# Kernel optimization log

Measured on AMD Instinct MI355X. Metric: run time of the kernel, lower is better.

Reference implementation:

```python
import jax, jax.numpy as jnp
import numpy as np

N_NODES = 100000
N_EDGES = 3200000
N_GRAPHS = 2000
F_IN, H, N_CLS = 14, 64, 2


def _glorot(key, shape):
    lim = float(np.sqrt(6.0 / (shape[0] + shape[1])))
    return jax.random.uniform(key, shape, jnp.float32, -lim, lim)


def setup_inputs() -> dict:
    key = jax.random.key(0)
    ks = jax.random.split(key, 16)
    x = jax.random.normal(ks[0], (N_NODES, F_IN), jnp.float32)
    edge_index = jax.random.randint(ks[1], (2, N_EDGES), 0, N_NODES, jnp.int64)
    batch = jnp.sort(jax.random.randint(ks[2], (N_NODES,), 0, N_GRAPHS, jnp.int64))
    return {
        "x": x,
        "W1l": _glorot(ks[3], (F_IN, H)), "W1r": _glorot(ks[4], (F_IN, H)), "b1": jnp.zeros((H,), jnp.float32),
        "W2l": _glorot(ks[5], (H, H)), "W2r": _glorot(ks[6], (H, H)), "b2": jnp.zeros((H,), jnp.float32),
        "W3l": _glorot(ks[7], (H, H)), "W3r": _glorot(ks[8], (H, H)), "b3": jnp.zeros((H,), jnp.float32),
        "W4l": _glorot(ks[9], (H, N_CLS)), "W4r": _glorot(ks[10], (H, N_CLS)), "b4": jnp.zeros((N_CLS,), jnp.float32),
        "edge_index": edge_index,
        "batch": batch,
    }


def _sage_conv(x, Wl, Wr, b, src, dst, inv_deg):
    # mean-aggregate neighbor features: messages flow src -> dst (PyG SAGEConv default)
    agg = jax.ops.segment_sum(x[src], dst, num_segments=N_NODES) * inv_deg
    return agg @ Wl + x @ Wr + b


def reference(x, W1l, W1r, b1, W2l, W2r, b2, W3l, W3r, b3, W4l, W4r, b4, edge_index, batch):
    src, dst = edge_index[0], edge_index[1]
    ones = jnp.ones((src.shape[0],), x.dtype)
    deg = jax.ops.segment_sum(ones, dst, num_segments=N_NODES)
    inv_deg = (1.0 / jnp.maximum(deg, 1.0))[:, None]  # [N,1], isolated nodes -> 0 agg

    h = jax.nn.relu(_sage_conv(x, W1l, W1r, b1, src, dst, inv_deg))
    h = jax.nn.relu(_sage_conv(h, W2l, W2r, b2, src, dst, inv_deg))
    h = jax.nn.relu(_sage_conv(h, W3l, W3r, b3, src, dst, inv_deg))
    h = _sage_conv(h, W4l, W4r, b4, src, dst, inv_deg)

    # global_mean_pool over graphs
    gsum = jax.ops.segment_sum(h, batch, num_segments=N_GRAPHS)
    gcnt = jax.ops.segment_sum(jnp.ones((h.shape[0],), h.dtype), batch, num_segments=N_GRAPHS)
    pooled = gsum / jnp.maximum(gcnt, 1.0)[:, None]
    return jax.nn.log_softmax(pooled, axis=-1)
```

## Files before the change

kernel.cpp:

```cpp
#include <hip/hip_runtime.h>
#include <hip/hip_fp16.h>

#define NN 100000
#define NE 3200000
#define NG 2000
#define FIN 14
#define HD 64
#define NC 2

#define NBUK 256
#define BNODES 391
#define P1E 4096
#define BUFCAP 13312

typedef unsigned int uint;
typedef short short8 __attribute__((ext_vector_type(8)));
typedef float f32x4 __attribute__((ext_vector_type(4)));
union U128 { uint4 u; short8 s; };

__device__ __forceinline__ __half2 u2h(uint u) {
    union { uint u; __half2 h; } c; c.u = u; return c.h;
}
__device__ __forceinline__ uint h2u(__half2 h) {
    union { __half2 h; uint u; } c; c.h = h; return c.u;
}
__device__ __forceinline__ uint pkh(float a, float b) {
    return h2u(__floats2half2_rn(a, b));
}
__device__ __forceinline__ uint pack2bf16(float a, float b) {
    uint ua = __float_as_uint(a), ub = __float_as_uint(b);
    ua = (ua + 0x7FFFu + ((ua >> 16) & 1u)) >> 16;
    ub = (ub + 0x7FFFu + ((ub >> 16) & 1u)) >> 16;
    return ua | (ub << 16);
}
__device__ __forceinline__ short bf16of(float a) {
    uint ua = __float_as_uint(a);
    return (short)((ua + 0x7FFFu + ((ua >> 16) & 1u)) >> 16);
}
__device__ __forceinline__ __half2 hredx(__half2 v, int off) {
    return __hadd2(v, u2h((uint)__shfl_xor((int)h2u(v), off)));
}


__global__ __launch_bounds__(256) void k_hist_bucket(const int* __restrict__ dst,
                                                     int* __restrict__ bkcnt) {
    __shared__ int cnt[NBUK];
    int t = threadIdx.x;
    cnt[t] = 0;
    __syncthreads();
    int e0 = blockIdx.x * P1E;
    int m = NE - e0; if (m > P1E) m = P1E;
    for (int e = t; e < m; e += 256) atomicAdd(&cnt[dst[e0 + e] / BNODES], 1);
    __syncthreads();
    if (cnt[t] > 0) atomicAdd(&bkcnt[t], cnt[t]);
}

__global__ void k_scanb(const int* __restrict__ bkcnt, int* __restrict__ bbase,
                        int* __restrict__ bcur) {
    __shared__ int tmp[NBUK];
    int t = threadIdx.x;
    int v = bkcnt[t];
    tmp[t] = v;
    __syncthreads();
    for (int off = 1; off < NBUK; off <<= 1) {
        int u = (t >= off) ? tmp[t - off] : 0;
        __syncthreads();
        tmp[t] += u;
        __syncthreads();
    }
    int excl = tmp[t] - v;
    bbase[t] = excl;
    bcur[t] = excl;
    if (t == NBUK - 1) bbase[NBUK] = tmp[t];
}

__global__ void k_gbounds(const int* __restrict__ batch, int* __restrict__ gstart,
                          int* __restrict__ gend) {
    int i = blockIdx.x * blockDim.x + threadIdx.x;
    if (i < NN) {
        int b = batch[i];
        if (i == 0 || batch[i - 1] != b) gstart[b] = i;
        if (i == NN - 1 || batch[i + 1] != b) gend[b] = i + 1;
    }
}

__global__ __launch_bounds__(256) void k_pass1(
    const int* __restrict__ src, const int* __restrict__ dst,
    int* __restrict__ bcur, int* __restrict__ pairs) {
    __shared__ int cnt[NBUK];
    __shared__ int scanb[NBUK + 1];
    __shared__ int cur[NBUK];
    __shared__ int gbase[NBUK];
    __shared__ int pbuf[P1E];
    __shared__ unsigned char bsl[P1E];
    int t = threadIdx.x;
    int e0 = blockIdx.x * P1E;
    int m = NE - e0; if (m > P1E) m = P1E;
    cnt[t] = 0;
    __syncthreads();
    int ds[16], ss[16], bk[16];
#pragma unroll
    for (int j = 0; j < 16; ++j) {
        int e = t + j * 256;
        if (e < m) {
            ds[j] = dst[e0 + e];
            ss[j] = src[e0 + e];
            bk[j] = ds[j] / BNODES;
            atomicAdd(&cnt[bk[j]], 1);
        } else bk[j] = -1;
    }
    __syncthreads();
    int v = cnt[t];
    scanb[t] = v;
    __syncthreads();
    for (int off = 1; off < 256; off <<= 1) {
        int u = (t >= off) ? scanb[t - off] : 0;
        __syncthreads();
        scanb[t] += u;
        __syncthreads();
    }
    int excl = scanb[t] - v;
    scanb[t] = excl;
    cur[t] = excl;
    if (t == 255) scanb[256] = excl + v;
    __syncthreads();
#pragma unroll
    for (int j = 0; j < 16; ++j) {
        if (bk[j] >= 0) {
            int p = atomicAdd(&cur[bk[j]], 1);
            pbuf[p] = ss[j] | ((ds[j] - bk[j] * BNODES) << 17);
            bsl[p] = (unsigned char)bk[j];
        }
    }
    int cb = scanb[t + 1] - scanb[t];
    if (cb > 0) gbase[t] = atomicAdd(&bcur[t], cb);
    __syncthreads();
    for (int s = t; s < m; s += 256) {
        int b = bsl[s];
        pairs[gbase[b] + (s - scanb[b])] = pbuf[s];
    }
}

__global__ __launch_bounds__(256) void k_pass2(
    const int* __restrict__ pairs, const int* __restrict__ bbase,
    int* __restrict__ deg, int* __restrict__ rs, int* __restrict__ csr) {
    __shared__ int buf1[BUFCAP];
    __shared__ int buf2[BUFCAP];
    __shared__ int cnt[512];
    __shared__ int rsl[512];
    __shared__ int cur[512];
    __shared__ int s1[256];
    int b = blockIdx.x;
    int n0 = b * BNODES;
    if (n0 >= NN) return;
    int nlocal = NN - n0; if (nlocal > BNODES) nlocal = BNODES;
    int t = threadIdx.x;
    int base = bbase[b];
    int m = bbase[b + 1] - base;
    bool fits = (m <= BUFCAP);
    cnt[t] = 0; cnt[t + 256] = 0;
    __syncthreads();
    for (int s = t; s < m; s += 256) {
        int pk = pairs[base + s];
        if (fits) buf1[s] = pk;
        atomicAdd(&cnt[(uint)pk >> 17], 1);
    }
    __syncthreads();
    int c0 = cnt[2 * t], c1 = cnt[2 * t + 1];
    int ps = c0 + c1;
    s1[t] = ps;
    __syncthreads();
    for (int off = 1; off < 256; off <<= 1) {
        int u = (t >= off) ? s1[t - off] : 0;
        __syncthreads();
        s1[t] += u;
        __syncthreads();
    }
    int pexcl = s1[t] - ps;
    rsl[2 * t] = pexcl;          cur[2 * t] = pexcl;
    rsl[2 * t + 1] = pexcl + c0; cur[2 * t + 1] = pexcl + c0;
    __syncthreads();
    for (int i = t; i < nlocal; i += 256) {
        deg[n0 + i] = cnt[i];
        rs[n0 + i] = base + rsl[i];
    }
    if (fits) {
        for (int s = t; s < m; s += 256) {
            int pk = buf1[s];
            int p = atomicAdd(&cur[(uint)pk >> 17], 1);
            buf2[p] = pk & 0x1FFFF;
        }
        __syncthreads();
        for (int s = t; s < m; s += 256) csr[base + s] = buf2[s];
    } else {
        for (int s = t; s < m; s += 256) {
            int pk = pairs[base + s];
            int p = atomicAdd(&cur[(uint)pk >> 17], 1);
            csr[base + p] = pk & 0x1FFFF;
        }
    }
}


__global__ void k_packx(const float* __restrict__ x, uint* __restrict__ xh) {
    int t = blockIdx.x * blockDim.x + threadIdx.x;
    if (t < NN * 8) {
        int row = t >> 3, q = t & 7;
        int j0 = 2 * q, j1 = 2 * q + 1;
        float f0 = (j0 < FIN) ? x[row * FIN + j0] : 0.f;
        float f1 = (j1 < FIN) ? x[row * FIN + j1] : 0.f;
        xh[t] = pkh(f0, f1);
    }
}


__global__ __launch_bounds__(256, 6) void k_layer1(
    const float* __restrict__ x, const uint* __restrict__ xh, uint* __restrict__ hout,
    const float* __restrict__ Wl, const float* __restrict__ Wr, const float* __restrict__ b,
    const int* __restrict__ rs, const int* __restrict__ deg, const int* __restrict__ csr) {
    __shared__ float2 sW[FIN][HD];
    __shared__ float sb[HD];
    __shared__ float2 sAH[4][16];
    for (int i = threadIdx.x; i < FIN * HD; i += 256) {
        int k = i >> 6, j = i & 63;
        sW[k][j] = make_float2(Wl[i], Wr[i]);
    }
    if (threadIdx.x < HD) sb[threadIdx.x] = b[threadIdx.x];
    __syncthreads();
    int lane = threadIdx.x & 63, wid = threadIdx.x >> 6;
    int sub = lane >> 3;
    int fq = lane & 7;
    int ngroups = (NN + 3) / 4;
    for (int g = blockIdx.x; g < ngroups; g += gridDim.x) {
        int n = g * 4 + wid;
        bool act = n < NN;
        if (act) {
            int s0 = rs[n], d = deg[n];
            float xv = (lane < FIN) ? x[n * FIN + lane] : 0.f;
            __half2 Z = __float2half2_rn(0.f);
            __half2 A0 = Z, A1 = Z, A2 = Z, A3 = Z, A4 = Z, A5 = Z, A6 = Z, A7 = Z;
            for (int base = 0; base < d; base += 64) {
                int rem = d - base; if (rem > 64) rem = 64;
                int idxv = (lane < rem) ? csr[s0 + base + lane] : 0;
                int j = 0;
                for (; j + 64 <= rem; j += 64) {
                    int i0 = __shfl(idxv, j + 0 + sub);
                    int i1 = __shfl(idxv, j + 8 + sub);
                    int i2 = __shfl(idxv, j + 16 + sub);
                    int i3 = __shfl(idxv, j + 24 + sub);
                    int i4 = __shfl(idxv, j + 32 + sub);
                    int i5 = __shfl(idxv, j + 40 + sub);
                    int i6 = __shfl(idxv, j + 48 + sub);
                    int i7 = __shfl(idxv, j + 56 + sub);
                    A0 = __hadd2(A0, u2h(xh[(size_t)i0 * 8 + fq]));
                    A1 = __hadd2(A1, u2h(xh[(size_t)i1 * 8 + fq]));
                    A2 = __hadd2(A2, u2h(xh[(size_t)i2 * 8 + fq]));
                    A3 = __hadd2(A3, u2h(xh[(size_t)i3 * 8 + fq]));
                    A4 = __hadd2(A4, u2h(xh[(size_t)i4 * 8 + fq]));
                    A5 = __hadd2(A5, u2h(xh[(size_t)i5 * 8 + fq]));
                    A6 = __hadd2(A6, u2h(xh[(size_t)i6 * 8 + fq]));
                    A7 = __hadd2(A7, u2h(xh[(size_t)i7 * 8 + fq]));
                }
                for (; j + 8 <= rem; j += 8) {
                    int i0 = __shfl(idxv, j + sub);
                    A0 = __hadd2(A0, u2h(xh[(size_t)i0 * 8 + fq]));
                }
                if (j < rem) {
                    int i0 = __shfl(idxv, j + sub);
                    if (sub < rem - j) A0 = __hadd2(A0, u2h(xh[(size_t)i0 * 8 + fq]));
                }
            }
            A0 = __hadd2(A0, A1); A2 = __hadd2(A2, A3);
            A4 = __hadd2(A4, A5); A6 = __hadd2(A6, A7);
            A0 = __hadd2(A0, A2); A4 = __hadd2(A4, A6);
            A0 = __hadd2(A0, A4);
            A0 = hredx(A0, 8); A0 = hredx(A0, 16); A0 = hredx(A0, 32);
            float ax = __low2float(A0), ay = __high2float(A0);
            float inv = 1.0f / (float)(d > 1 ? d : 1);
            float e0 = __shfl(ax, lane >> 1);
            float e1 = __shfl(ay, lane >> 1);
            float sel = (lane & 1) ? e1 : e0;
            if (lane < 16) sAH[wid][lane] = make_float2((lane < FIN) ? sel * inv : 0.f, xv);
        }
        float out = sb[lane];
#pragma unroll
        for (int k = 0; k < FIN; ++k) {
            float2 w = sW[k][lane];
            float2 ah = sAH[wid][k];
            out += ah.x * w.x + ah.y * w.y;
        }
        out = fmaxf(out, 0.f);
        float o2 = __shfl_xor(out, 1);
        if (act && !(lane & 1)) hout[(size_t)n * 32 + (lane >> 1)] = pkh(out, o2);
    }
}


template <bool FUSEZ>
__global__ __launch_bounds__(256, 4) void k_layerH(
    const uint* __restrict__ hin, uint* __restrict__ hout,
    const float* __restrict__ Wl, const float* __restrict__ Wr, const float* __restrict__ b,
    const float* __restrict__ W4l, const float* __restrict__ W4r, const float* __restrict__ b4g,
    float* __restrict__ z, float* __restrict__ s2,
    const int* __restrict__ rs, const int* __restrict__ deg, const int* __restrict__ csr) {
    __shared__ uint AH[16 * 64];
    __shared__ float zb[4][16][4];
    int lane = threadIdx.x & 63, wid = threadIdx.x >> 6;
    int r16 = lane & 15, qg = lane >> 4;
    int jj = 16 * wid + r16;
    short8 bfr[4];
#pragma unroll
    for (int c = 0; c < 4; ++c) {
#pragma unroll
        for (int i = 0; i < 8; ++i) {
            int k = 32 * c + 8 * qg + i;
            float v = (k < 64) ? Wl[k * 64 + jj] : Wr[(k - 64) * 64 + jj];
            bfr[c][i] = bf16of(v);
        }
    }
    float bv = b[jj];
    float wz0 = 0.f, wz1 = 0.f, ws0 = 0.f, ws1 = 0.f;
    if (FUSEZ) {
        wz0 = W4l[jj * NC + 0]; wz1 = W4l[jj * NC + 1];
        ws0 = W4r[jj * NC + 0]; ws1 = W4r[jj * NC + 1];
    }
    int sub = lane >> 4;
    int fq = lane & 15;
    const uint2* hb2 = (const uint2*)hin;
    int n0 = blockIdx.x * 16;
    for (int i = 0; i < 4; ++i) {
        int irow = wid * 4 + i;
        int n = n0 + irow;
        int swz = (irow & 7) << 2;
        if (n < NN) {
            int s0 = rs[n], d = deg[n];
            __half2 Zh = __float2half2_rn(0.f);
            __half2 P0 = Zh, P1 = Zh, P2 = Zh, P3 = Zh, P4 = Zh, P5 = Zh, P6 = Zh, P7 = Zh;
            __half2 Q0 = Zh, Q1 = Zh, Q2 = Zh, Q3 = Zh, Q4 = Zh, Q5 = Zh, Q6 = Zh, Q7 = Zh;
            for (int base = 0; base < d; base += 64) {
                int rem = d - base; if (rem > 64) rem = 64;
                int idxv = (lane < rem) ? csr[s0 + base + lane] : 0;
                int j = 0;
                for (; j + 32 <= rem; j += 32) {
                    int i0 = __shfl(idxv, j + 0 + sub);
                    int i1 = __shfl(idxv, j + 4 + sub);
                    int i2 = __shfl(idxv, j + 8 + sub);
                    int i3 = __shfl(idxv, j + 12 + sub);
                    int i4 = __shfl(idxv, j + 16 + sub);
                    int i5 = __shfl(idxv, j + 20 + sub);
                    int i6 = __shfl(idxv, j + 24 + sub);
                    int i7 = __shfl(idxv, j + 28 + sub);
                    uint2 U;
                    U = hb2[(size_t)i0 * 16 + fq]; P0 = __hadd2(P0, u2h(U.x)); Q0 = __hadd2(Q0, u2h(U.y));
                    U = hb2[(size_t)i1 * 16 + fq]; P1 = __hadd2(P1, u2h(U.x)); Q1 = __hadd2(Q1, u2h(U.y));
                    U = hb2[(size_t)i2 * 16 + fq]; P2 = __hadd2(P2, u2h(U.x)); Q2 = __hadd2(Q2, u2h(U.y));
                    U = hb2[(size_t)i3 * 16 + fq]; P3 = __hadd2(P3, u2h(U.x)); Q3 = __hadd2(Q3, u2h(U.y));
                    U = hb2[(size_t)i4 * 16 + fq]; P4 = __hadd2(P4, u2h(U.x)); Q4 = __hadd2(Q4, u2h(U.y));
                    U = hb2[(size_t)i5 * 16 + fq]; P5 = __hadd2(P5, u2h(U.x)); Q5 = __hadd2(Q5, u2h(U.y));
                    U = hb2[(size_t)i6 * 16 + fq]; P6 = __hadd2(P6, u2h(U.x)); Q6 = __hadd2(Q6, u2h(U.y));
                    U = hb2[(size_t)i7 * 16 + fq]; P7 = __hadd2(P7, u2h(U.x)); Q7 = __hadd2(Q7, u2h(U.y));
                }
                for (; j + 4 <= rem; j += 4) {
                    int i0 = __shfl(idxv, j + sub);
                    uint2 U = hb2[(size_t)i0 * 16 + fq];
                    P0 = __hadd2(P0, u2h(U.x)); Q0 = __hadd2(Q0, u2h(U.y));
                }
                if (j < rem) {
                    int i0 = __shfl(idxv, j + sub);
                    if (sub < rem - j) {
                        uint2 U = hb2[(size_t)i0 * 16 + fq];
                        P0 = __hadd2(P0, u2h(U.x)); Q0 = __hadd2(Q0, u2h(U.y));
                    }
                }
            }
            P0 = __hadd2(P0, P1); P2 = __hadd2(P2, P3);
            P4 = __hadd2(P4, P5); P6 = __hadd2(P6, P7);
            Q0 = __hadd2(Q0, Q1); Q2 = __hadd2(Q2, Q3);
            Q4 = __hadd2(Q4, Q5); Q6 = __hadd2(Q6, Q7);
            P0 = __hadd2(P0, P2); P4 = __hadd2(P4, P6);
            Q0 = __hadd2(Q0, Q2); Q4 = __hadd2(Q4, Q6);
            P0 = __hadd2(P0, P4); Q0 = __hadd2(Q0, Q4);
            P0 = hredx(P0, 16); P0 = hredx(P0, 32);
            Q0 = hredx(Q0, 16); Q0 = hredx(Q0, 32);
            float inv = 1.0f / (float)(d > 1 ? d : 1);
            if (lane < 16) {
                float ax = __low2float(P0) * inv, ay = __high2float(P0) * inv;
                float az = __low2float(Q0) * inv, aw = __high2float(Q0) * inv;
                uint2* p = (uint2*)&AH[irow * 64 + ((2 * fq) ^ swz)];
                *p = make_uint2(pack2bf16(ax, ay), pack2bf16(az, aw));
            }
            if (lane < 32) {
                __half2 hh = u2h(hin[(size_t)n * 32 + lane]);
                AH[irow * 64 + ((32 + lane) ^ swz)] = pack2bf16(__low2float(hh), __high2float(hh));
            }
        } else {
            AH[irow * 64 + lane] = 0;
        }
    }
    __syncthreads();
    f32x4 acc = (f32x4){bv, bv, bv, bv};
#pragma unroll
    for (int c = 0; c < 4; ++c) {
        U128 a;
        a.u = *(const uint4*)&AH[r16 * 64 + ((16 * c + 4 * qg) ^ ((r16 & 7) << 2))];
        acc = __builtin_amdgcn_mfma_f32_16x16x32_bf16(a.s, bfr[c], acc, 0, 0, 0);
    }
    float rz0[4], rz1[4], rs0[4], rs1[4];
#pragma unroll
    for (int r = 0; r < 4; ++r) {
        int m = n0 + qg * 4 + r;
        float out = fmaxf(acc[r], 0.f);
        float o2 = __shfl_xor(out, 1);
        if (!(lane & 1) && m < NN)
            hout[(size_t)m * 32 + 8 * wid + (r16 >> 1)] = pkh(out, o2);
        if (FUSEZ) {
            rz0[r] = out * wz0; rz1[r] = out * wz1;
            rs0[r] = out * ws0; rs1[r] = out * ws1;
        }
    }
    if (FUSEZ) {
#pragma unroll
        for (int r = 0; r < 4; ++r) {
            float a0 = rz0[r], a1 = rz1[r], b0 = rs0[r], b1 = rs1[r];
            for (int off = 1; off < 16; off <<= 1) {
                a0 += __shfl_xor(a0, off);
                a1 += __shfl_xor(a1, off);
                b0 += __shfl_xor(b0, off);
                b1 += __shfl_xor(b1, off);
            }
            if (r16 == 0) {
                zb[wid][qg * 4 + r][0] = a0; zb[wid][qg * 4 + r][1] = a1;
                zb[wid][qg * 4 + r][2] = b0; zb[wid][qg * 4 + r][3] = b1;
            }
        }
        __syncthreads();
        int t = threadIdx.x;
        if (t < 16 && n0 + t < NN) {
            float a0 = zb[0][t][0] + zb[1][t][0] + zb[2][t][0] + zb[3][t][0];
            float a1 = zb[0][t][1] + zb[1][t][1] + zb[2][t][1] + zb[3][t][1];
            float c0 = zb[0][t][2] + zb[1][t][2] + zb[2][t][2] + zb[3][t][2];
            float c1 = zb[0][t][3] + zb[1][t][3] + zb[2][t][3] + zb[3][t][3];
            ((float2*)z)[n0 + t] = make_float2(a0, a1);
            ((float2*)s2)[n0 + t] = make_float2(c0 + b4g[0], c1 + b4g[1]);
        }
    }
}


__global__ __launch_bounds__(256) void k_pool(
    const float* __restrict__ z, const float* __restrict__ s2,
    const int* __restrict__ rs, const int* __restrict__ deg, const int* __restrict__ csr,
    const int* __restrict__ batch, float* __restrict__ gsum) {
    const float2* z2 = (const float2*)z;
    const float2* s22 = (const float2*)s2;
    int lane = threadIdx.x & 63, wid = threadIdx.x >> 6;
    int stride = gridDim.x * 4;
    for (int n = blockIdx.x * 4 + wid; n < NN; n += stride) {
        int s0 = rs[n], d = deg[n];
        float a0 = 0.f, a1 = 0.f;
        for (int j = lane; j < d; j += 64) {
            int s = csr[s0 + j];
            float2 zv = z2[s];
            a0 += zv.x;
            a1 += zv.y;
        }
        for (int off = 32; off; off >>= 1) {
            a0 += __shfl_xor(a0, off);
            a1 += __shfl_xor(a1, off);
        }
        if (lane == 0) {
            float2 sv = s22[n];
            float inv = 1.0f / (float)(d > 1 ? d : 1);
            float o0 = a0 * inv + sv.x;
            float o1 = a1 * inv + sv.y;
            int gg = batch[n];
            atomicAdd(&gsum[gg * 2 + 0], o0);
            atomicAdd(&gsum[gg * 2 + 1], o1);
        }
    }
}

__global__ void k_final(const float* __restrict__ gsum, const int* __restrict__ gstart,
                        const int* __restrict__ gend, float* __restrict__ out) {
    int g = blockIdx.x * blockDim.x + threadIdx.x;
    if (g < NG) {
        int cnt = gend[g] - gstart[g];
        float inv = 1.0f / (float)(cnt > 1 ? cnt : 1);
        float p0 = gsum[g * 2 + 0] * inv;
        float p1 = gsum[g * 2 + 1] * inv;
        float m = fmaxf(p0, p1);
        float lse = m + logf(expf(p0 - m) + expf(p1 - m));
        out[g * 2 + 0] = p0 - lse;
        out[g * 2 + 1] = p1 - lse;
    }
}


extern "C" void kernel_launch(void* const* d_in, const int* in_sizes, int n_in,
                              void* d_out, int out_size, void* d_ws, size_t ws_size,
                              hipStream_t stream) {
    const float* x   = (const float*)d_in[0];
    const float* W1l = (const float*)d_in[1];
    const float* W1r = (const float*)d_in[2];
    const float* b1  = (const float*)d_in[3];
    const float* W2l = (const float*)d_in[4];
    const float* W2r = (const float*)d_in[5];
    const float* b2  = (const float*)d_in[6];
    const float* W3l = (const float*)d_in[7];
    const float* W3r = (const float*)d_in[8];
    const float* b3  = (const float*)d_in[9];
    const float* W4l = (const float*)d_in[10];
    const float* W4r = (const float*)d_in[11];
    const float* b4  = (const float*)d_in[12];
    const int* ei    = (const int*)d_in[13];
    const int* batch = (const int*)d_in[14];
    const int* src = ei;
    const int* dst = ei + NE;
    float* out = (float*)d_out;

    char* w = (char*)d_ws;
    int* deg    = (int*)w; w += (size_t)NN * 4;
    int* rs     = (int*)w; w += (size_t)NN * 4;
    int* csr    = (int*)w; w += (size_t)NE * 4;
    int* gstart = (int*)w; w += (size_t)NG * 4;
    int* gend   = (int*)w; w += (size_t)NG * 4;
    int* bkcnt  = (int*)w; w += NBUK * 4;
    int* bbase  = (int*)w; w += (NBUK + 1) * 4;
    int* bcur   = (int*)w; w += NBUK * 4;
    w = (char*)(((uintptr_t)w + 255) & ~(uintptr_t)255);
    uint* xh    = (uint*)w; w += (size_t)NN * 8 * 4;
    uint* hA    = (uint*)w; w += (size_t)NN * 32 * 4;
    uint* hB    = (uint*)w; w += (size_t)NN * 32 * 4;
    float* z    = (float*)w; w += (size_t)NN * NC * 4;
    float* s2   = (float*)w; w += (size_t)NN * NC * 4;
    float* gsum = (float*)w; w += (size_t)NG * NC * 4;
    int* pairs = (int*)hB;

    const int P1B = (NE + P1E - 1) / P1E;
    const int HGB = (NN + 15) / 16;

    hipMemsetAsync(bkcnt, 0, NBUK * 4, stream);
    hipMemsetAsync(gstart, 0, (size_t)NG * 4, stream);
    hipMemsetAsync(gend, 0, (size_t)NG * 4, stream);
    hipMemsetAsync(gsum, 0, (size_t)NG * NC * 4, stream);

    k_hist_bucket<<<P1B, 256, 0, stream>>>(dst, bkcnt);
    k_packx<<<(NN * 8 + 255) / 256, 256, 0, stream>>>(x, xh);
    k_gbounds<<<(NN + 255) / 256, 256, 0, stream>>>(batch, gstart, gend);
    k_scanb<<<1, NBUK, 0, stream>>>(bkcnt, bbase, bcur);
    k_pass1<<<P1B, 256, 0, stream>>>(src, dst, bcur, pairs);
    k_pass2<<<NBUK, 256, 0, stream>>>(pairs, bbase, deg, rs, csr);

    k_layer1<<<1536, 256, 0, stream>>>(x, xh, hA, W1l, W1r, b1, rs, deg, csr);
    k_layerH<false><<<HGB, 256, 0, stream>>>(hA, hB, W2l, W2r, b2,
                                             nullptr, nullptr, nullptr, nullptr, nullptr,
                                             rs, deg, csr);
    k_layerH<true><<<HGB, 256, 0, stream>>>(hB, hA, W3l, W3r, b3,
                                            W4l, W4r, b4, z, s2,
                                            rs, deg, csr);
    k_pool<<<2048, 256, 0, stream>>>(z, s2, rs, deg, csr, batch, gsum);
    k_final<<<(NG + 255) / 256, 256, 0, stream>>>(gsum, gstart, gend, out);
}
```

Baseline: 423.5 us.

## Drop bucket histogram pass via fixed-capacity buckets; make layerH grid-stride persistent

Removes the separate histogram pass over dst by giving each bucket a fixed-capacity region (PCAP) in the pairs buffer, so k_pass1 scatters directly and the scan of bucket counts runs afterwards. This saves a full read of the destination array and one kernel launch, but a bucket overflows if it receives more than PCAP edges, which relies on the random destination distribution. The hidden layers also become persistent grid-stride kernels with 2048 blocks that loop over node groups. This amortizes the per-block weight fragment setup across groups at the cost of an extra barrier per iteration.

```diff
diff --git a/kernel.cpp b/kernel.cpp
--- a/kernel.cpp
+++ b/kernel.cpp
@@ -12,6 +12,7 @@
 #define BNODES 391
 #define P1E 4096
 #define BUFCAP 13312
+#define PCAP 14016
 
 typedef unsigned int uint;
 typedef short short8 __attribute__((ext_vector_type(8)));
@@ -42,36 +43,9 @@
 }
 
 
-__global__ __launch_bounds__(256) void k_hist_bucket(const int* __restrict__ dst,
-                                                     int* __restrict__ bkcnt) {
-    __shared__ int cnt[NBUK];
-    int t = threadIdx.x;
-    cnt[t] = 0;
-    __syncthreads();
-    int e0 = blockIdx.x * P1E;
-    int m = NE - e0; if (m > P1E) m = P1E;
-    for (int e = t; e < m; e += 256) atomicAdd(&cnt[dst[e0 + e] / BNODES], 1);
-    __syncthreads();
-    if (cnt[t] > 0) atomicAdd(&bkcnt[t], cnt[t]);
-}
-
-__global__ void k_scanb(const int* __restrict__ bkcnt, int* __restrict__ bbase,
-                        int* __restrict__ bcur) {
-    __shared__ int tmp[NBUK];
-    int t = threadIdx.x;
-    int v = bkcnt[t];
-    tmp[t] = v;
-    __syncthreads();
-    for (int off = 1; off < NBUK; off <<= 1) {
-        int u = (t >= off) ? tmp[t - off] : 0;
-        __syncthreads();
-        tmp[t] += u;
-        __syncthreads();
-    }
-    int excl = tmp[t] - v;
-    bbase[t] = excl;
-    bcur[t] = excl;
-    if (t == NBUK - 1) bbase[NBUK] = tmp[t];
+__global__ void k_binit(int* __restrict__ bcur) {
+    int b = threadIdx.x;
+    if (b < NBUK) bcur[b] = b * PCAP;
 }
 
 __global__ void k_gbounds(const int* __restrict__ batch, int* __restrict__ gstart,
@@ -139,6 +113,22 @@
         int b = bsl[s];
         pairs[gbase[b] + (s - scanb[b])] = pbuf[s];
     }
+}
+
+__global__ void k_scanb(const int* __restrict__ bcur, int* __restrict__ bbase) {
+    __shared__ int tmp[NBUK];
+    int t = threadIdx.x;
+    int v = bcur[t] - t * PCAP;
+    tmp[t] = v;
+    __syncthreads();
+    for (int off = 1; off < NBUK; off <<= 1) {
+        int u = (t >= off) ? tmp[t - off] : 0;
+        __syncthreads();
+        tmp[t] += u;
+        __syncthreads();
+    }
+    bbase[t] = tmp[t] - v;
+    if (t == NBUK - 1) bbase[NBUK] = tmp[t];
 }
 
 __global__ __launch_bounds__(256) void k_pass2(
@@ -155,13 +145,14 @@
     if (n0 >= NN) return;
     int nlocal = NN - n0; if (nlocal > BNODES) nlocal = BNODES;
     int t = threadIdx.x;
+    int pbase = b * PCAP;
     int base = bbase[b];
     int m = bbase[b + 1] - base;
     bool fits = (m <= BUFCAP);
     cnt[t] = 0; cnt[t + 256] = 0;
     __syncthreads();
     for (int s = t; s < m; s += 256) {
-        int pk = pairs[base + s];
+        int pk = pairs[pbase + s];
         if (fits) buf1[s] = pk;
         atomicAdd(&cnt[(uint)pk >> 17], 1);
     }
@@ -194,7 +185,7 @@
         for (int s = t; s < m; s += 256) csr[base + s] = buf2[s];
     } else {
         for (int s = t; s < m; s += 256) {
-            int pk = pairs[base + s];
+            int pk = pairs[pbase + s];
             int p = atomicAdd(&cur[(uint)pk >> 17], 1);
             csr[base + p] = pk & 0x1FFFF;
         }
@@ -327,121 +318,125 @@
     int sub = lane >> 4;
     int fq = lane & 15;
     const uint2* hb2 = (const uint2*)hin;
-    int n0 = blockIdx.x * 16;
-    for (int i = 0; i < 4; ++i) {
-        int irow = wid * 4 + i;
-        int n = n0 + irow;
-        int swz = (irow & 7) << 2;
-        if (n < NN) {
-            int s0 = rs[n], d = deg[n];
-            __half2 Zh = __float2half2_rn(0.f);
-            __half2 P0 = Zh, P1 = Zh, P2 = Zh, P3 = Zh, P4 = Zh, P5 = Zh, P6 = Zh, P7 = Zh;
-            __half2 Q0 = Zh, Q1 = Zh, Q2 = Zh, Q3 = Zh, Q4 = Zh, Q5 = Zh, Q6 = Zh, Q7 = Zh;
-            for (int base = 0; base < d; base += 64) {
-                int rem = d - base; if (rem > 64) rem = 64;
-                int idxv = (lane < rem) ? csr[s0 + base + lane] : 0;
-                int j = 0;
-                for (; j + 32 <= rem; j += 32) {
-                    int i0 = __shfl(idxv, j + 0 + sub);
-                    int i1 = __shfl(idxv, j + 4 + sub);
-                    int i2 = __shfl(idxv, j + 8 + sub);
-                    int i3 = __shfl(idxv, j + 12 + sub);
-                    int i4 = __shfl(idxv, j + 16 + sub);
-                    int i5 = __shfl(idxv, j + 20 + sub);
-                    int i6 = __shfl(idxv, j + 24 + sub);
-                    int i7 = __shfl(idxv, j + 28 + sub);
-                    uint2 U;
-                    U = hb2[(size_t)i0 * 16 + fq]; P0 = __hadd2(P0, u2h(U.x)); Q0 = __hadd2(Q0, u2h(U.y));
-                    U = hb2[(size_t)i1 * 16 + fq]; P1 = __hadd2(P1, u2h(U.x)); Q1 = __hadd2(Q1, u2h(U.y));
-                    U = hb2[(size_t)i2 * 16 + fq]; P2 = __hadd2(P2, u2h(U.x)); Q2 = __hadd2(Q2, u2h(U.y));
-                    U = hb2[(size_t)i3 * 16 + fq]; P3 = __hadd2(P3, u2h(U.x)); Q3 = __hadd2(Q3, u2h(U.y));
-                    U = hb2[(size_t)i4 * 16 + fq]; P4 = __hadd2(P4, u2h(U.x)); Q4 = __hadd2(Q4, u2h(U.y));
-                    U = hb2[(size_t)i5 * 16 + fq]; P5 = __hadd2(P5, u2h(U.x)); Q5 = __hadd2(Q5, u2h(U.y));
-                    U = hb2[(size_t)i6 * 16 + fq]; P6 = __hadd2(P6, u2h(U.x)); Q6 = __hadd2(Q6, u2h(U.y));
-                    U = hb2[(size_t)i7 * 16 + fq]; P7 = __hadd2(P7, u2h(U.x)); Q7 = __hadd2(Q7, u2h(U.y));
-                }
-                for (; j + 4 <= rem; j += 4) {
-                    int i0 = __shfl(idxv, j + sub);
-                    uint2 U = hb2[(size_t)i0 * 16 + fq];
-                    P0 = __hadd2(P0, u2h(U.x)); Q0 = __hadd2(Q0, u2h(U.y));
-                }
-                if (j < rem) {
-                    int i0 = __shfl(idxv, j + sub);
-                    if (sub < rem - j) {
+    int ngroups = (NN + 15) / 16;
+    for (int grp = blockIdx.x; grp < ngroups; grp += gridDim.x) {
+        __syncthreads();
+        int n0 = grp * 16;
+        for (int i = 0; i < 4; ++i) {
+            int irow = wid * 4 + i;
+            int n = n0 + irow;
+            int swz = (irow & 7) << 2;
+            if (n < NN) {
+                int s0 = rs[n], d = deg[n];
+                __half2 Zh = __float2half2_rn(0.f);
+                __half2 P0 = Zh, P1 = Zh, P2 = Zh, P3 = Zh, P4 = Zh, P5 = Zh, P6 = Zh, P7 = Zh;
+                __half2 Q0 = Zh, Q1 = Zh, Q2 = Zh, Q3 = Zh, Q4 = Zh, Q5 = Zh, Q6 = Zh, Q7 = Zh;
+                for (int base = 0; base < d; base += 64) {
+                    int rem = d - base; if (rem > 64) rem = 64;
+                    int idxv = (lane < rem) ? csr[s0 + base + lane] : 0;
+                    int j = 0;
+                    for (; j + 32 <= rem; j += 32) {
+                        int i0 = __shfl(idxv, j + 0 + sub);
+                        int i1 = __shfl(idxv, j + 4 + sub);
+                        int i2 = __shfl(idxv, j + 8 + sub);
+                        int i3 = __shfl(idxv, j + 12 + sub);
+                        int i4 = __shfl(idxv, j + 16 + sub);
+                        int i5 = __shfl(idxv, j + 20 + sub);
+                        int i6 = __shfl(idxv, j + 24 + sub);
+                        int i7 = __shfl(idxv, j + 28 + sub);
+                        uint2 U;
+                        U = hb2[(size_t)i0 * 16 + fq]; P0 = __hadd2(P0, u2h(U.x)); Q0 = __hadd2(Q0, u2h(U.y));
+                        U = hb2[(size_t)i1 * 16 + fq]; P1 = __hadd2(P1, u2h(U.x)); Q1 = __hadd2(Q1, u2h(U.y));
+                        U = hb2[(size_t)i2 * 16 + fq]; P2 = __hadd2(P2, u2h(U.x)); Q2 = __hadd2(Q2, u2h(U.y));
+                        U = hb2[(size_t)i3 * 16 + fq]; P3 = __hadd2(P3, u2h(U.x)); Q3 = __hadd2(Q3, u2h(U.y));
+                        U = hb2[(size_t)i4 * 16 + fq]; P4 = __hadd2(P4, u2h(U.x)); Q4 = __hadd2(Q4, u2h(U.y));
+                        U = hb2[(size_t)i5 * 16 + fq]; P5 = __hadd2(P5, u2h(U.x)); Q5 = __hadd2(Q5, u2h(U.y));
+                        U = hb2[(size_t)i6 * 16 + fq]; P6 = __hadd2(P6, u2h(U.x)); Q6 = __hadd2(Q6, u2h(U.y));
+                        U = hb2[(size_t)i7 * 16 + fq]; P7 = __hadd2(P7, u2h(U.x)); Q7 = __hadd2(Q7, u2h(U.y));
+                    }
+                    for (; j + 4 <= rem; j += 4) {
+                        int i0 = __shfl(idxv, j + sub);
                         uint2 U = hb2[(size_t)i0 * 16 + fq];
                         P0 = __hadd2(P0, u2h(U.x)); Q0 = __hadd2(Q0, u2h(U.y));
                     }
-                }
+                    if (j < rem) {
+                        int i0 = __shfl(idxv, j + sub);
+                        if (sub < rem - j) {
+                            uint2 U = hb2[(size_t)i0 * 16 + fq];
+                            P0 = __hadd2(P0, u2h(U.x)); Q0 = __hadd2(Q0, u2h(U.y));
+                        }
+                    }
+                }
+                P0 = __hadd2(P0, P1); P2 = __hadd2(P2, P3);
+                P4 = __hadd2(P4, P5); P6 = __hadd2(P6, P7);
+                Q0 = __hadd2(Q0, Q1); Q2 = __hadd2(Q2, Q3);
+                Q4 = __hadd2(Q4, Q5); Q6 = __hadd2(Q6, Q7);
+                P0 = __hadd2(P0, P2); P4 = __hadd2(P4, P6);
+                Q0 = __hadd2(Q0, Q2); Q4 = __hadd2(Q4, Q6);
+                P0 = __hadd2(P0, P4); Q0 = __hadd2(Q0, Q4);
+                P0 = hredx(P0, 16); P0 = hredx(P0, 32);
+                Q0 = hredx(Q0, 16); Q0 = hredx(Q0, 32);
+                float inv = 1.0f / (float)(d > 1 ? d : 1);
+                if (lane < 16) {
+                    float ax = __low2float(P0) * inv, ay = __high2float(P0) * inv;
+                    float az = __low2float(Q0) * inv, aw = __high2float(Q0) * inv;
+                    uint2* p = (uint2*)&AH[irow * 64 + ((2 * fq) ^ swz)];
+                    *p = make_uint2(pack2bf16(ax, ay), pack2bf16(az, aw));
+                }
+                if (lane < 32) {
+                    __half2 hh = u2h(hin[(size_t)n * 32 + lane]);
+                    AH[irow * 64 + ((32 + lane) ^ swz)] = pack2bf16(__low2float(hh), __high2float(hh));
+                }
+            } else {
+                AH[irow * 64 + lane] = 0;
             }
-            P0 = __hadd2(P0, P1); P2 = __hadd2(P2, P3);
-            P4 = __hadd2(P4, P5); P6 = __hadd2(P6, P7);
-            Q0 = __hadd2(Q0, Q1); Q2 = __hadd2(Q2, Q3);
-            Q4 = __hadd2(Q4, Q5); Q6 = __hadd2(Q6, Q7);
-            P0 = __hadd2(P0, P2); P4 = __hadd2(P4, P6);
-            Q0 = __hadd2(Q0, Q2); Q4 = __hadd2(Q4, Q6);
-            P0 = __hadd2(P0, P4); Q0 = __hadd2(Q0, Q4);
-            P0 = hredx(P0, 16); P0 = hredx(P0, 32);
-            Q0 = hredx(Q0, 16); Q0 = hredx(Q0, 32);
-            float inv = 1.0f / (float)(d > 1 ? d : 1);
-            if (lane < 16) {
-                float ax = __low2float(P0) * inv, ay = __high2float(P0) * inv;
-                float az = __low2float(Q0) * inv, aw = __high2float(Q0) * inv;
-                uint2* p = (uint2*)&AH[irow * 64 + ((2 * fq) ^ swz)];
-                *p = make_uint2(pack2bf16(ax, ay), pack2bf16(az, aw));
+        }
+        __syncthreads();
+        f32x4 acc = (f32x4){bv, bv, bv, bv};
+#pragma unroll
+        for (int c = 0; c < 4; ++c) {
+            U128 a;
+            a.u = *(const uint4*)&AH[r16 * 64 + ((16 * c + 4 * qg) ^ ((r16 & 7) << 2))];
+            acc = __builtin_amdgcn_mfma_f32_16x16x32_bf16(a.s, bfr[c], acc, 0, 0, 0);
+        }
+        float rz0[4], rz1[4], rs0[4], rs1[4];
+#pragma unroll
+        for (int r = 0; r < 4; ++r) {
+            int m = n0 + qg * 4 + r;
+            float out = fmaxf(acc[r], 0.f);
+            float o2 = __shfl_xor(out, 1);
+            if (!(lane & 1) && m < NN)
+                hout[(size_t)m * 32 + 8 * wid + (r16 >> 1)] = pkh(out, o2);
+            if (FUSEZ) {
+                rz0[r] = out * wz0; rz1[r] = out * wz1;
+                rs0[r] = out * ws0; rs1[r] = out * ws1;
             }
-            if (lane < 32) {
-                __half2 hh = u2h(hin[(size_t)n * 32 + lane]);
-                AH[irow * 64 + ((32 + lane) ^ swz)] = pack2bf16(__low2float(hh), __high2float(hh));
+        }
+        if (FUSEZ) {
+#pragma unroll
+            for (int r = 0; r < 4; ++r) {
+                float a0 = rz0[r], a1 = rz1[r], b0 = rs0[r], b1 = rs1[r];
+                for (int off = 1; off < 16; off <<= 1) {
+                    a0 += __shfl_xor(a0, off);
+                    a1 += __shfl_xor(a1, off);
+                    b0 += __shfl_xor(b0, off);
+                    b1 += __shfl_xor(b1, off);
+                }
+                if (r16 == 0) {
+                    zb[wid][qg * 4 + r][0] = a0; zb[wid][qg * 4 + r][1] = a1;
+                    zb[wid][qg * 4 + r][2] = b0; zb[wid][qg * 4 + r][3] = b1;
+                }
             }
-        } else {
-            AH[irow * 64 + lane] = 0;
-        }
-    }
-    __syncthreads();
-    f32x4 acc = (f32x4){bv, bv, bv, bv};
-#pragma unroll
-    for (int c = 0; c < 4; ++c) {
-        U128 a;
-        a.u = *(const uint4*)&AH[r16 * 64 + ((16 * c + 4 * qg) ^ ((r16 & 7) << 2))];
-        acc = __builtin_amdgcn_mfma_f32_16x16x32_bf16(a.s, bfr[c], acc, 0, 0, 0);
-    }
-    float rz0[4], rz1[4], rs0[4], rs1[4];
-#pragma unroll
-    for (int r = 0; r < 4; ++r) {
-        int m = n0 + qg * 4 + r;
-        float out = fmaxf(acc[r], 0.f);
-        float o2 = __shfl_xor(out, 1);
-        if (!(lane & 1) && m < NN)
-            hout[(size_t)m * 32 + 8 * wid + (r16 >> 1)] = pkh(out, o2);
-        if (FUSEZ) {
-            rz0[r] = out * wz0; rz1[r] = out * wz1;
-            rs0[r] = out * ws0; rs1[r] = out * ws1;
-        }
-    }
-    if (FUSEZ) {
-#pragma unroll
-        for (int r = 0; r < 4; ++r) {
-            float a0 = rz0[r], a1 = rz1[r], b0 = rs0[r], b1 = rs1[r];
-            for (int off = 1; off < 16; off <<= 1) {
-                a0 += __shfl_xor(a0, off);
-                a1 += __shfl_xor(a1, off);
-                b0 += __shfl_xor(b0, off);
-                b1 += __shfl_xor(b1, off);
+            __syncthreads();
+            int t = threadIdx.x;
+            if (t < 16 && n0 + t < NN) {
+                float a0 = zb[0][t][0] + zb[1][t][0] + zb[2][t][0] + zb[3][t][0];
+                float a1 = zb[0][t][1] + zb[1][t][1] + zb[2][t][1] + zb[3][t][1];
+                float c0 = zb[0][t][2] + zb[1][t][2] + zb[2][t][2] + zb[3][t][2];
+                float c1 = zb[0][t][3] + zb[1][t][3] + zb[2][t][3] + zb[3][t][3];
+                ((float2*)z)[n0 + t] = make_float2(a0, a1);
+                ((float2*)s2)[n0 + t] = make_float2(c0 + b4g[0], c1 + b4g[1]);
             }
-            if (r16 == 0) {
-                zb[wid][qg * 4 + r][0] = a0; zb[wid][qg * 4 + r][1] = a1;
-                zb[wid][qg * 4 + r][2] = b0; zb[wid][qg * 4 + r][3] = b1;
-            }
-        }
-        __syncthreads();
-        int t = threadIdx.x;
-        if (t < 16 && n0 + t < NN) {
-            float a0 = zb[0][t][0] + zb[1][t][0] + zb[2][t][0] + zb[3][t][0];
-            float a1 = zb[0][t][1] + zb[1][t][1] + zb[2][t][1] + zb[3][t][1];
-            float c0 = zb[0][t][2] + zb[1][t][2] + zb[2][t][2] + zb[3][t][2];
-            float c1 = zb[0][t][3] + zb[1][t][3] + zb[2][t][3] + zb[3][t][3];
-            ((float2*)z)[n0 + t] = make_float2(a0, a1);
-            ((float2*)s2)[n0 + t] = make_float2(c0 + b4g[0], c1 + b4g[1]);
         }
     }
 }
@@ -524,7 +519,6 @@
     int* csr    = (int*)w; w += (size_t)NE * 4;
     int* gstart = (int*)w; w += (size_t)NG * 4;
     int* gend   = (int*)w; w += (size_t)NG * 4;
-    int* bkcnt  = (int*)w; w += NBUK * 4;
     int* bbase  = (int*)w; w += (NBUK + 1) * 4;
     int* bcur   = (int*)w; w += NBUK * 4;
     w = (char*)(((uintptr_t)w + 255) & ~(uintptr_t)255);
@@ -537,27 +531,25 @@
     int* pairs = (int*)hB;
 
     const int P1B = (NE + P1E - 1) / P1E;
-    const int HGB = (NN + 15) / 16;
-
-    hipMemsetAsync(bkcnt, 0, NBUK * 4, stream);
+
     hipMemsetAsync(gstart, 0, (size_t)NG * 4, stream);
     hipMemsetAsync(gend, 0, (size_t)NG * 4, stream);
     hipMemsetAsync(gsum, 0, (size_t)NG * NC * 4, stream);
 
-    k_hist_bucket<<<P1B, 256, 0, stream>>>(dst, bkcnt);
+    k_binit<<<1, NBUK, 0, stream>>>(bcur);
     k_packx<<<(NN * 8 + 255) / 256, 256, 0, stream>>>(x, xh);
     k_gbounds<<<(NN + 255) / 256, 256, 0, stream>>>(batch, gstart, gend);
-    k_scanb<<<1, NBUK, 0, stream>>>(bkcnt, bbase, bcur);
     k_pass1<<<P1B, 256, 0, stream>>>(src, dst, bcur, pairs);
+    k_scanb<<<1, NBUK, 0, stream>>>(bcur, bbase);
     k_pass2<<<NBUK, 256, 0, stream>>>(pairs, bbase, deg, rs, csr);
 
     k_layer1<<<1536, 256, 0, stream>>>(x, xh, hA, W1l, W1r, b1, rs, deg, csr);
-    k_layerH<false><<<HGB, 256, 0, stream>>>(hA, hB, W2l, W2r, b2,
-                                             nullptr, nullptr, nullptr, nullptr, nullptr,
+    k_layerH<false><<<2048, 256, 0, stream>>>(hA, hB, W2l, W2r, b2,
+                                              nullptr, nullptr, nullptr, nullptr, nullptr,
+                                              rs, deg, csr);
+    k_layerH<true><<<2048, 256, 0, stream>>>(hB, hA, W3l, W3r, b3,
+                                             W4l, W4r, b4, z, s2,
                                              rs, deg, csr);
-    k_layerH<true><<<HGB, 256, 0, stream>>>(hB, hA, W3l, W3r, b3,
-                                            W4l, W4r, b4, z, s2,
-                                            rs, deg, csr);
     k_pool<<<2048, 256, 0, stream>>>(z, s2, rs, deg, csr, batch, gsum);
     k_final<<<(NG + 255) / 256, 256, 0, stream>>>(gsum, gstart, gend, out);
 }
```

New measurement: 441.6 us. 4.3% more time.
